# Performance work log

Measured on AMD Instinct MI355X. Metric: run time of the kernel, lower is better.

The kernel has to match this reference:

```python
import jax, jax.numpy as jnp
import numpy as np

NU, NS, NM = 80000, 20000, 30000
D = 128
E_UI, E_MM = 1_500_000, 480_000
B, L = 2048, 32
LAYERS = 2


def spmm(rows, cols, vals, x, n):
    # sparse [n,n] @ dense [n,d] via gather + segment_sum
    return jax.ops.segment_sum(vals[:, None] * x[cols], rows, num_segments=n)


def setup_inputs() -> dict:
    key = jax.random.key(0)
    ks = jax.random.split(key, 20)
    inp = {}
    inp['mashup_inputs'] = jax.random.randint(ks[0], (B,), 0, NM, dtype=jnp.int32)
    inp['service_inputs'] = jax.random.randint(ks[1], (B,), 0, NS, dtype=jnp.int32)
    inp['member_masked'] = jax.random.randint(ks[2], (B, L), 0, NU, dtype=jnp.int32)
    # variable-length compose lists: length in [1, L]; mask==1 marks padding
    lens = jax.random.randint(ks[3], (B, 1), 1, L + 1)
    inp['mask'] = (jnp.arange(L)[None, :] >= lens).astype(jnp.float32)
    inp['member_masked'] = jnp.where(inp['mask'] > 0, 0, inp['member_masked'])
    inp['adj_rows'] = jax.random.randint(ks[4], (E_UI,), 0, NU + NS, dtype=jnp.int32)
    inp['adj_cols'] = jax.random.randint(ks[5], (E_UI,), 0, NU + NS, dtype=jnp.int32)
    inp['adj_vals'] = jax.random.uniform(ks[6], (E_UI,)) * 0.1
    inp['A_rows'] = jax.random.randint(ks[7], (E_MM,), 0, NM, dtype=jnp.int32)
    inp['A_cols'] = jax.random.randint(ks[8], (E_MM,), 0, NM, dtype=jnp.int32)
    inp['A_vals'] = jax.random.uniform(ks[9], (E_MM,)) * 0.1
    inp['d_inv'] = jax.random.uniform(ks[10], (NM,)) * 0.1
    s = 0.05
    inp['user_tbl'] = jax.random.normal(ks[11], (NU, D)) * s
    inp['service_tbl'] = jax.random.normal(ks[12], (NS, D)) * s
    inp['mashup_tbl'] = jax.random.normal(ks[13], (NM, D)) * s
    inp['att_w1'] = jax.random.normal(ks[14], (2 * D, 16)) * s
    inp['att_b1'] = jnp.zeros((16,))
    inp['att_w2'] = jax.random.normal(ks[15], (16, 1)) * s
    inp['att_b2'] = jnp.zeros((1,))
    inp['pred_w1'] = jax.random.normal(ks[16], (3 * D, 8)) * s
    inp['pred_b1'] = jnp.zeros((8,))
    inp['pred_w2'] = jax.random.normal(ks[17], (8, 1)) * s
    inp['pred_b2'] = jnp.zeros((1,))
    return inp


def reference(mashup_inputs, service_inputs, member_masked, adj_rows, adj_cols,
              A_rows, A_cols, mask, user_tbl, service_tbl, mashup_tbl,
              adj_vals, A_vals, d_inv, att_w1, att_b1, att_w2, att_b2,
              pred_w1, pred_b1, pred_w2, pred_b2):
    # HyperConv on concatenated user+service embeddings (layer-mean aggregation)
    ui = jnp.concatenate([user_tbl, service_tbl], axis=0)  # [NU+NS, D]
    acc, h = ui, ui
    for _ in range(LAYERS):
        h = spmm(adj_rows, adj_cols, adj_vals, h, NU + NS)
        acc = acc + h
    ui = acc / (LAYERS + 1)
    user_e, service_e = ui[:NU], ui[NU:]
    service_emb = service_e[service_inputs]  # [B, D]

    # HyperConv2 on mashup graph: emb <- D^-1 A emb per layer, layer-mean
    acc, m = mashup_tbl, mashup_tbl
    for _ in range(LAYERS):
        m = d_inv[:, None] * spmm(A_rows, A_cols, A_vals, m, NM)
        acc = acc + m
    mashup_embedding = acc / (LAYERS + 1)

    # ragged gather + masked attention pooling over compose members
    member_emb = user_e[member_masked]                      # [B, L, D]
    svc_exp = jnp.broadcast_to(service_emb[:, None, :], (B, L, D))
    at_emb = jnp.concatenate([member_emb, svc_exp], axis=2)  # [B, L, 2D]
    hdn = jax.nn.relu(at_emb @ att_w1 + att_b1)             # [B, L, 16]
    scores = (hdn @ att_w2 + att_b2)[..., 0]                 # [B, L]
    scores = jnp.where(mask > 0, -1e9, scores)               # mask padding
    at_wt = jax.nn.softmax(scores, axis=1)
    g_att = jnp.einsum('bl,bld->bd', at_wt, member_emb)      # [B, D]

    mashup_emb = g_att + mashup_embedding[mashup_inputs]
    elem = mashup_emb * service_emb
    new_emb = jnp.concatenate([elem, mashup_emb, service_emb], axis=1)  # [B, 3D]
    hp = jax.nn.relu(new_emb @ pred_w1 + pred_b1)
    y = jax.nn.sigmoid(hp @ pred_w2 + pred_b2)               # [B, 1]
    return y
```

## Files before the change

kernel.cpp:

```cpp
#include <hip/hip_runtime.h>
#include <climits>

#define NU_ 80000
#define NS_ 20000
#define NM_ 30000
#define UIN_ (NU_ + NS_)
#define DD 128
#define LL 32
#define RPB 64
#define NCH 256
#define NBUK_UI ((UIN_ + RPB - 1) / RPB)
#define NBUK_MM ((NM_  + RPB - 1) / RPB)

#define F8_SCALE 512.0f
#define F8_INV   (1.0f / 512.0f)

typedef unsigned int   uint32;
typedef unsigned short ushort_t;
typedef unsigned char  uchar_t;
typedef float f32x2 __attribute__((ext_vector_type(2)));

__device__ __forceinline__ float bflo(uint32 u) { return __uint_as_float(u << 16); }
__device__ __forceinline__ float bfhi(uint32 u) { return __uint_as_float(u & 0xffff0000u); }
__device__ __forceinline__ uint32 f2bf(float f) {
    uint32 u = __float_as_uint(f);
    return (u + 0x7fffu + ((u >> 16) & 1u)) >> 16;
}
__device__ __forceinline__ uint32 pack2bf(float lo, float hi) {
    return f2bf(lo) | (f2bf(hi) << 16);
}

__device__ __forceinline__ float dec1_f8(uint32 b) {
    uint32 em = b & 0x7fu;
    uint32 s  = (b & 0x80u) << 24;
    float vn = __uint_as_float(s | (((em >> 3) + 120u) << 23) | ((em & 7u) << 20));
    float vd = (float)(int)em * 0.001953125f;
    vd = (b & 0x80u) ? -vd : vd;
    return (em >= 8u) ? vn : vd;
}
__device__ __forceinline__ uint32 enc1_f8(float f) {
    uint32 u = __float_as_uint(f);
    uint32 s = (u >> 31) << 7;
    float a = fabsf(f);
    if (a >= 448.0f) return s | 0x7Eu;
    if (a < 0.015625f) {
        int m = (int)(a * 512.0f + 0.5f);
        return s | (uint32)m;
    }
    uint32 au = u & 0x7fffffffu;
    au += 0x7FFFFu + ((au >> 20) & 1u);
    uint32 em = (((au >> 23) - 120u) << 3) | ((au >> 20) & 7u);
    if (em >= 0x7Fu) em = 0x7Eu;
    return s | em;
}
__device__ __forceinline__ f32x2 dec2_f8(uint32 u) {
#if __has_builtin(__builtin_amdgcn_cvt_pk_f32_fp8)
    return __builtin_amdgcn_cvt_pk_f32_fp8(u, false);
#else
    f32x2 r; r.x = dec1_f8(u & 0xffu); r.y = dec1_f8((u >> 8) & 0xffu); return r;
#endif
}
__device__ __forceinline__ f32x2 dec2_f8_hi(uint32 u) {
#if __has_builtin(__builtin_amdgcn_cvt_pk_f32_fp8)
    return __builtin_amdgcn_cvt_pk_f32_fp8(u, true);
#else
    f32x2 r; r.x = dec1_f8((u >> 16) & 0xffu); r.y = dec1_f8(u >> 24); return r;
#endif
}
__device__ __forceinline__ uint32 pack2f8(float lo, float hi) {
#if __has_builtin(__builtin_amdgcn_cvt_pk_fp8_f32)
    return (uint32)__builtin_amdgcn_cvt_pk_fp8_f32(lo, hi, 0, false) & 0xFFFFu;
#else
    return enc1_f8(lo) | (enc1_f8(hi) << 8);
#endif
}

__global__ void convert_kernel(const float* __restrict__ srcA, const float* __restrict__ srcB,
                               int split_rows, uint32* __restrict__ dst_bf,
                               ushort_t* __restrict__ dst_f8, size_t n2) {
    size_t stride = (size_t)gridDim.x * blockDim.x;
    const size_t split_e = (size_t)split_rows * DD;
    for (size_t i = (size_t)blockIdx.x * blockDim.x + threadIdx.x; i < n2; i += stride) {
        size_t e = i * 2;
        const float* s = (e < split_e) ? (srcA + e) : (srcB + (e - split_e));
        float2 v = *reinterpret_cast<const float2*>(s);
        dst_bf[i] = pack2bf(v.x, v.y);
        dst_f8[i] = (ushort_t)pack2f8(v.x * F8_SCALE, v.y * F8_SCALE);
    }
}

template <int NBUK>
__global__ __launch_bounds__(1024) void bucket_histA(const int* __restrict__ rows, int E,
                                                     int csz, int* __restrict__ h) {
    __shared__ int hist[NBUK];
    for (int i = threadIdx.x; i < NBUK; i += 1024) hist[i] = 0;
    __syncthreads();
    const int c  = blockIdx.x;
    const int lo = c * csz, hi = min(lo + csz, E);
    int i = lo + threadIdx.x;
    for (; i + 3 * 1024 < hi; i += 4 * 1024) {
        int r0 = rows[i];
        int r1 = rows[i + 1024];
        int r2 = rows[i + 2048];
        int r3 = rows[i + 3072];
        atomicAdd(&hist[r0 >> 6], 1);
        atomicAdd(&hist[r1 >> 6], 1);
        atomicAdd(&hist[r2 >> 6], 1);
        atomicAdd(&hist[r3 >> 6], 1);
    }
    for (; i < hi; i += 1024) atomicAdd(&hist[rows[i] >> 6], 1);
    __syncthreads();
    for (int b = threadIdx.x; b < NBUK; b += 1024)
        h[b * NCH + c] = hist[b];
}

__global__ __launch_bounds__(256) void scan_blocksum(const int* __restrict__ cnt,
                                                     int* __restrict__ bsum, int n) {
    __shared__ int red[256];
    int base = blockIdx.x * 1024 + threadIdx.x * 4;
    int s = 0;
    if (base + 3 < n) {
        int4 v = *reinterpret_cast<const int4*>(cnt + base);
        s = v.x + v.y + v.z + v.w;
    } else {
        for (int i = base; i < n && i < base + 4; ++i) s += cnt[i];
    }
    red[threadIdx.x] = s;
    __syncthreads();
    for (int off = 128; off >= 1; off >>= 1) {
        if (threadIdx.x < off) red[threadIdx.x] += red[threadIdx.x + off];
        __syncthreads();
    }
    if (threadIdx.x == 0) bsum[blockIdx.x] = red[0];
}

__global__ __launch_bounds__(256) void scan_final(const int* __restrict__ cnt,
                                                  const int* __restrict__ bsum,
                                                  int* __restrict__ row_ptr,
                                                  int* __restrict__ cursor, int n) {
    __shared__ int lds[256];
    __shared__ int blk_off_s;
    const int tid = threadIdx.x;
    const int b   = blockIdx.x;

    int s = 0;
    for (int j = tid; j < b; j += 256) s += bsum[j];
    lds[tid] = s;
    __syncthreads();
    for (int off = 128; off >= 1; off >>= 1) {
        if (tid < off) lds[tid] += lds[tid + off];
        __syncthreads();
    }
    if (tid == 0) blk_off_s = lds[0];
    __syncthreads();
    const int blk_off = blk_off_s;

    int base = b * 1024 + tid * 4;
    int c0 = 0, c1 = 0, c2 = 0, c3 = 0;
    if (base + 3 < n) {
        int4 v = *reinterpret_cast<const int4*>(cnt + base);
        c0 = v.x; c1 = v.y; c2 = v.z; c3 = v.w;
    } else {
        if (base     < n) c0 = cnt[base];
        if (base + 1 < n) c1 = cnt[base + 1];
        if (base + 2 < n) c2 = cnt[base + 2];
        if (base + 3 < n) c3 = cnt[base + 3];
    }
    int tsum = c0 + c1 + c2 + c3;
    __syncthreads();
    lds[tid] = tsum;
    __syncthreads();
    for (int off = 1; off < 256; off <<= 1) {
        int v = (tid >= off) ? lds[tid - off] : 0;
        __syncthreads();
        lds[tid] += v;
        __syncthreads();
    }
    int p0 = blk_off + ((tid > 0) ? lds[tid - 1] : 0);
    int p1 = p0 + c0, p2 = p1 + c1, p3 = p2 + c2, p4 = p3 + c3;

    if (base     < n) { row_ptr[base]     = p0; cursor[base]     = p0; if (base     == n - 1) row_ptr[n] = p1; }
    if (base + 1 < n) { row_ptr[base + 1] = p1; cursor[base + 1] = p1; if (base + 1 == n - 1) row_ptr[n] = p2; }
    if (base + 2 < n) { row_ptr[base + 2] = p2; cursor[base + 2] = p2; if (base + 2 == n - 1) row_ptr[n] = p3; }
    if (base + 3 < n) { row_ptr[base + 3] = p3; cursor[base + 3] = p3; if (base + 3 == n - 1) row_ptr[n] = p4; }
}

template <int NBUK>
__global__ __launch_bounds__(1024) void bucket_scatterA(
    const int* __restrict__ rows, const int* __restrict__ cols,
    const float* __restrict__ vals, const int* __restrict__ s,
    int E, int csz, uint2* __restrict__ cvA) {
    __shared__ int cur[NBUK];
    const int c = blockIdx.x;
    for (int b = threadIdx.x; b < NBUK; b += 1024) cur[b] = s[b * NCH + c];
    __syncthreads();
    const int lo = c * csz, hi = min(lo + csz, E);
    int i = lo + threadIdx.x;
    for (; i + 3 * 1024 < hi; i += 4 * 1024) {
        int   r0 = rows[i],        r1 = rows[i + 1024];
        int   r2 = rows[i + 2048], r3 = rows[i + 3072];
        int   q0 = cols[i],        q1 = cols[i + 1024];
        int   q2 = cols[i + 2048], q3 = cols[i + 3072];
        float v0 = vals[i],        v1 = vals[i + 1024];
        float v2 = vals[i + 2048], v3 = vals[i + 3072];
        int p0 = atomicAdd(&cur[r0 >> 6], 1);
        int p1 = atomicAdd(&cur[r1 >> 6], 1);
        int p2 = atomicAdd(&cur[r2 >> 6], 1);
        int p3 = atomicAdd(&cur[r3 >> 6], 1);
        cvA[p0] = make_uint2((uint32)q0 | ((uint32)(r0 & 63) << 25), __float_as_uint(v0));
        cvA[p1] = make_uint2((uint32)q1 | ((uint32)(r1 & 63) << 25), __float_as_uint(v1));
        cvA[p2] = make_uint2((uint32)q2 | ((uint32)(r2 & 63) << 25), __float_as_uint(v2));
        cvA[p3] = make_uint2((uint32)q3 | ((uint32)(r3 & 63) << 25), __float_as_uint(v3));
    }
    for (; i < hi; i += 1024) {
        int r = rows[i];
        int pos = atomicAdd(&cur[r >> 6], 1);
        cvA[pos] = make_uint2((uint32)cols[i] | ((uint32)(r & 63) << 25),
                              __float_as_uint(vals[i]));
    }
}

__global__ __launch_bounds__(256) void sort_bucket(
    const uint2* __restrict__ cvA, const int* __restrict__ s,
    uint2* __restrict__ cvB, int* __restrict__ row_ptr, int nrows) {
    __shared__ int cnt[RPB];
    __shared__ int cur[RPB];
    const int b    = blockIdx.x;
    const int tid  = threadIdx.x;
    const int base = s[b * NCH];
    const int endb = s[(b + 1) * NCH];

    if (tid < RPB) cnt[tid] = 0;
    __syncthreads();
    for (int i = base + tid; i < endb; i += 256)
        atomicAdd(&cnt[cvA[i].x >> 25], 1);
    __syncthreads();
    if (tid < 64) {
        int c = cnt[tid];
        int x = c;
        #pragma unroll
        for (int off = 1; off < 64; off <<= 1) {
            int v = __shfl_up(x, off);
            if (tid >= off) x += v;
        }
        int excl = base + x - c;
        cur[tid] = excl;
        int grow = b * RPB + tid;
        if (grow <= nrows) row_ptr[grow] = excl;
    }
    __syncthreads();
    for (int i = base + tid; i < endb; i += 256) {
        uint2 e = cvA[i];
        int rl  = (int)(e.x >> 25);
        int pos = atomicAdd(&cur[rl], 1);
        cvB[pos] = make_uint2(e.x & 0x1FFFFFFu, e.y);
    }
}

template <int MODE>
__global__ __launch_bounds__(256) void pull_kernel(
    const int* __restrict__ row_ptr, const uint2* __restrict__ cv,
    const uchar_t* __restrict__ x,
    const float* __restrict__ d_inv,
    const uint32* __restrict__ orig_bf, const uchar_t* __restrict__ hprev_f8,
    void* __restrict__ out, int n)
{
    const int wid  = (blockIdx.x * blockDim.x + threadIdx.x) >> 6;
    const int lane = threadIdx.x & 63;
    const int q    = lane >> 4;
    const int ql   = lane & 15;
    if (wid >= n) return;
    const int beg = row_ptr[wid];
    const int end = row_ptr[wid + 1];
    const int boff = ql << 3;

    float a0 = 0.f, a1 = 0.f, a2 = 0.f, a3 = 0.f;
    float a4 = 0.f, a5 = 0.f, a6 = 0.f, a7 = 0.f;

    int e = beg + q;
    for (; e + 4 < end; e += 8) {
        uint2 pa = cv[e];
        uint2 pb = cv[e + 4];
        uint2 ga = *reinterpret_cast<const uint2*>(x + (((size_t)pa.x) << 7) + boff);
        uint2 gb = *reinterpret_cast<const uint2*>(x + (((size_t)pb.x) << 7) + boff);
        float va = __uint_as_float(pa.y);
        float vb = __uint_as_float(pb.y);
        f32x2 d0 = dec2_f8(ga.x), d1 = dec2_f8_hi(ga.x);
        f32x2 d2 = dec2_f8(ga.y), d3 = dec2_f8_hi(ga.y);
        a0 += va * d0.x; a1 += va * d0.y; a2 += va * d1.x; a3 += va * d1.y;
        a4 += va * d2.x; a5 += va * d2.y; a6 += va * d3.x; a7 += va * d3.y;
        f32x2 e0 = dec2_f8(gb.x), e1 = dec2_f8_hi(gb.x);
        f32x2 e2 = dec2_f8(gb.y), e3 = dec2_f8_hi(gb.y);
        a0 += vb * e0.x; a1 += vb * e0.y; a2 += vb * e1.x; a3 += vb * e1.y;
        a4 += vb * e2.x; a5 += vb * e2.y; a6 += vb * e3.x; a7 += vb * e3.y;
    }
    if (e < end) {
        uint2 pa = cv[e];
        uint2 ga = *reinterpret_cast<const uint2*>(x + (((size_t)pa.x) << 7) + boff);
        float va = __uint_as_float(pa.y);
        f32x2 d0 = dec2_f8(ga.x), d1 = dec2_f8_hi(ga.x);
        f32x2 d2 = dec2_f8(ga.y), d3 = dec2_f8_hi(ga.y);
        a0 += va * d0.x; a1 += va * d0.y; a2 += va * d1.x; a3 += va * d1.y;
        a4 += va * d2.x; a5 += va * d2.y; a6 += va * d3.x; a7 += va * d3.y;
    }

    a0 += __shfl_xor(a0, 16); a0 += __shfl_xor(a0, 32);
    a1 += __shfl_xor(a1, 16); a1 += __shfl_xor(a1, 32);
    a2 += __shfl_xor(a2, 16); a2 += __shfl_xor(a2, 32);
    a3 += __shfl_xor(a3, 16); a3 += __shfl_xor(a3, 32);
    a4 += __shfl_xor(a4, 16); a4 += __shfl_xor(a4, 32);
    a5 += __shfl_xor(a5, 16); a5 += __shfl_xor(a5, 32);
    a6 += __shfl_xor(a6, 16); a6 += __shfl_xor(a6, 32);
    a7 += __shfl_xor(a7, 16); a7 += __shfl_xor(a7, 32);

    if (lane < 16) {
        if (MODE & 1) {
            float s = d_inv[wid];
            a0 *= s; a1 *= s; a2 *= s; a3 *= s;
            a4 *= s; a5 *= s; a6 *= s; a7 *= s;
        }
        if (MODE & 2) {
            const float inv3 = 1.0f / 3.0f;
            uint4 o = *reinterpret_cast<const uint4*>(orig_bf + (size_t)wid * 64 + (ql << 2));
            uint2 hp = *reinterpret_cast<const uint2*>(hprev_f8 + (((size_t)wid) << 7) + boff);
            f32x2 h0 = dec2_f8(hp.x), h1 = dec2_f8_hi(hp.x);
            f32x2 h2 = dec2_f8(hp.y), h3 = dec2_f8_hi(hp.y);
            uint4 r;
            r.x = pack2bf((bflo(o.x) + (h0.x + a0) * F8_INV) * inv3,
                          (bfhi(o.x) + (h0.y + a1) * F8_INV) * inv3);
            r.y = pack2bf((bflo(o.y) + (h1.x + a2) * F8_INV) * inv3,
                          (bfhi(o.y) + (h1.y + a3) * F8_INV) * inv3);
            r.z = pack2bf((bflo(o.z) + (h2.x + a4) * F8_INV) * inv3,
                          (bfhi(o.z) + (h2.y + a5) * F8_INV) * inv3);
            r.w = pack2bf((bflo(o.w) + (h3.x + a6) * F8_INV) * inv3,
                          (bfhi(o.w) + (h3.y + a7) * F8_INV) * inv3);
            *reinterpret_cast<uint4*>(reinterpret_cast<uint32*>(out) + (size_t)wid * 64 + (ql << 2)) = r;
        } else {
            uint2 r;
            r.x = pack2f8(a0, a1) | (pack2f8(a2, a3) << 16);
            r.y = pack2f8(a4, a5) | (pack2f8(a6, a7) << 16);
            *reinterpret_cast<uint2*>((uchar_t*)out + (((size_t)wid) << 7) + boff) = r;
        }
    }
}

__global__ __launch_bounds__(512) void attn_pred_kernel(
    const int* __restrict__ mashup_inputs, const int* __restrict__ service_inputs,
    const int* __restrict__ member_masked, const float* __restrict__ mask,
    const uint32* __restrict__ ui_final, const uint32* __restrict__ mash_final,
    const float* __restrict__ att_w1, const float* __restrict__ att_b1,
    const float* __restrict__ att_w2, const float* __restrict__ att_b2,
    const float* __restrict__ pred_w1, const float* __restrict__ pred_b1,
    const float* __restrict__ pred_w2, const float* __restrict__ pred_b2,
    float* __restrict__ out)
{
    const int b   = blockIdx.x;
    const int tid = threadIdx.x;

    __shared__ float mem_lds[LL * 129];
    __shared__ float svc_lds[DD];
    __shared__ float mash_lds[DD];
    __shared__ float w1_lds[2 * DD * 16];
    __shared__ float hdnw_lds[LL * 16];
    __shared__ float wt_lds[LL];
    __shared__ float new_lds[3 * DD];
    __shared__ float hp_lds[8];
    __shared__ int   midx[LL];

    if (tid < LL) midx[tid] = member_masked[b * LL + tid];
    for (int i = tid; i < 2 * DD * 16; i += 512) w1_lds[i] = att_w1[i];
    if (tid < 64) {
        int sidx = service_inputs[b];
        uint32 u = ui_final[(size_t)(NU_ + sidx) * 64 + tid];
        svc_lds[tid * 2]     = bflo(u);
        svc_lds[tid * 2 + 1] = bfhi(u);
    } else if (tid >= 448) {
        int t  = tid - 448;
        int mi = mashup_inputs[b];
        uint32 u = mash_final[(size_t)mi * 64 + t];
        mash_lds[t * 2]     = bflo(u);
        mash_lds[t * 2 + 1] = bfhi(u);
    }
    __syncthreads();

    for (int i = tid; i < LL * 64; i += 512) {
        int l = i >> 6, dp = (i & 63) * 2;
        uint32 u = ui_final[(size_t)midx[l] * 64 + (i & 63)];
        mem_lds[l * 129 + dp]     = bflo(u);
        mem_lds[l * 129 + dp + 1] = bfhi(u);
    }
    __syncthreads();

    {
        int l = tid >> 4, j = tid & 15;
        float acc = att_b1[j];
        const float* m = &mem_lds[l * 129];
        #pragma unroll 4
        for (int k = 0; k < DD; ++k) acc += m[k] * w1_lds[k * 16 + j];
        #pragma unroll 4
        for (int k = 0; k < DD; ++k) acc += svc_lds[k] * w1_lds[(DD + k) * 16 + j];
        acc = fmaxf(acc, 0.0f);
        hdnw_lds[l * 16 + j] = acc * att_w2[j];
    }
    __syncthreads();

    if (tid < 64) {
        float s = -3.0e38f;
        if (tid < LL) {
            s = att_b2[0];
            for (int j = 0; j < 16; ++j) s += hdnw_lds[tid * 16 + j];
            if (mask[b * LL + tid] > 0.0f) s = -1.0e9f;
        }
        float mx = s;
        for (int off = 16; off >= 1; off >>= 1) mx = fmaxf(mx, __shfl_xor(mx, off));
        float ex = (tid < LL) ? __expf(s - mx) : 0.0f;
        float sum = ex;
        for (int off = 16; off >= 1; off >>= 1) sum += __shfl_xor(sum, off);
        if (tid < LL) wt_lds[tid] = ex / sum;
    }
    __syncthreads();

    if (tid < DD) {
        float g = 0.0f;
        #pragma unroll 4
        for (int l = 0; l < LL; ++l) g += wt_lds[l] * mem_lds[l * 129 + tid];
        float me = g + mash_lds[tid];
        float sv = svc_lds[tid];
        new_lds[tid]          = me * sv;
        new_lds[DD + tid]     = me;
        new_lds[2 * DD + tid] = sv;
    }
    __syncthreads();

    if (tid < 8) {
        float acc = pred_b1[tid];
        for (int k = 0; k < 3 * DD; ++k) acc += new_lds[k] * pred_w1[k * 8 + tid];
        acc = fmaxf(acc, 0.0f);
        hp_lds[tid] = acc * pred_w2[tid];
    }
    __syncthreads();

    if (tid == 0) {
        float z = pred_b2[0];
        for (int j = 0; j < 8; ++j) z += hp_lds[j];
        out[b] = 1.0f / (1.0f + __expf(-z));
    }
}

extern "C" void kernel_launch(void* const* d_in, const int* in_sizes, int n_in,
                              void* d_out, int out_size, void* d_ws, size_t ws_size,
                              hipStream_t stream) {
    const int*   mashup_inputs  = (const int*)  d_in[0];
    const int*   service_inputs = (const int*)  d_in[1];
    const int*   member_masked  = (const int*)  d_in[2];
    const float* mask           = (const float*)d_in[3];
    const int*   adj_rows       = (const int*)  d_in[4];
    const int*   adj_cols       = (const int*)  d_in[5];
    const float* adj_vals       = (const float*)d_in[6];
    const int*   A_rows         = (const int*)  d_in[7];
    const int*   A_cols         = (const int*)  d_in[8];
    const float* A_vals         = (const float*)d_in[9];
    const float* d_inv          = (const float*)d_in[10];
    const float* user_tbl       = (const float*)d_in[11];
    const float* service_tbl    = (const float*)d_in[12];
    const float* mashup_tbl     = (const float*)d_in[13];
    const float* att_w1         = (const float*)d_in[14];
    const float* att_b1         = (const float*)d_in[15];
    const float* att_w2         = (const float*)d_in[16];
    const float* att_b2         = (const float*)d_in[17];
    const float* pred_w1        = (const float*)d_in[18];
    const float* pred_b1        = (const float*)d_in[19];
    const float* pred_w2        = (const float*)d_in[20];
    const float* pred_b2        = (const float*)d_in[21];

    const int E_ui = in_sizes[4];
    const int E_mm = in_sizes[7];
    const int B    = in_sizes[0];

    const int N_UI2  = NBUK_UI * NCH;
    const int N_MM2  = NBUK_MM * NCH;
    const int NB_UI  = (N_UI2 + 1023) / 1024;
    const int NB_MM  = (N_MM2 + 1023) / 1024;
    const int csz_ui = (E_ui + NCH - 1) / NCH;
    const int csz_mm = (E_mm + NCH - 1) / NCH;

    uint2*   cvA     = (uint2*)d_ws;
    uint2*   cvB_mm  = cvA + E_mm;
    uint2*   cvB_ui  = cvA + E_ui;
    int*     h_ui    = (int*)(cvB_ui + E_ui);
    int*     s_ui    = h_ui + N_UI2;
    int*     h_mm    = s_ui + N_UI2 + 4;
    int*     s_mm    = h_mm + N_MM2;
    int*     bs      = s_mm + N_MM2 + 4;
    int*     rp_ui   = bs + 512;
    int*     rp_mm   = rp_ui + UIN_ + 4;
    uint32*  ui_bf   = (uint32*)(rp_mm + NM_ + 4);
    uint32*  mash_bf = ui_bf + (size_t)UIN_ * 64;
    uint32*  h2      = mash_bf + (size_t)NM_ * 64;
    uint32*  m2      = h2 + (size_t)UIN_ * 64;
    uchar_t* ui_f8   = (uchar_t*)(m2 + (size_t)NM_ * 64);
    uchar_t* h1_f8   = ui_f8 + (size_t)UIN_ * DD;
    uchar_t* mash_f8 = h1_f8 + (size_t)UIN_ * DD;
    uchar_t* m1_f8   = mash_f8 + (size_t)NM_ * DD;

    convert_kernel<<<2048, 256, 0, stream>>>(user_tbl, service_tbl, NU_,
                                             ui_bf, (ushort_t*)ui_f8, (size_t)UIN_ * DD / 2);
    convert_kernel<<<1024, 256, 0, stream>>>(mashup_tbl, mashup_tbl, NM_,
                                             mash_bf, (ushort_t*)mash_f8, (size_t)NM_ * DD / 2);

    bucket_histA<NBUK_UI><<<NCH, 1024, 0, stream>>>(adj_rows, E_ui, csz_ui, h_ui);
    scan_blocksum<<<NB_UI, 256, 0, stream>>>(h_ui, bs, N_UI2);
    scan_final<<<NB_UI, 256, 0, stream>>>(h_ui, bs, s_ui, s_ui, N_UI2);
    bucket_scatterA<NBUK_UI><<<NCH, 1024, 0, stream>>>(adj_rows, adj_cols, adj_vals,
                                                       s_ui, E_ui, csz_ui, cvA);
    sort_bucket<<<NBUK_UI, 256, 0, stream>>>(cvA, s_ui, cvB_ui, rp_ui, UIN_);

    bucket_histA<NBUK_MM><<<NCH, 1024, 0, stream>>>(A_rows, E_mm, csz_mm, h_mm);
    scan_blocksum<<<NB_MM, 256, 0, stream>>>(h_mm, bs, N_MM2);
    scan_final<<<NB_MM, 256, 0, stream>>>(h_mm, bs, s_mm, s_mm, N_MM2);
    bucket_scatterA<NBUK_MM><<<NCH, 1024, 0, stream>>>(A_rows, A_cols, A_vals,
                                                       s_mm, E_mm, csz_mm, cvA);
    sort_bucket<<<NBUK_MM, 256, 0, stream>>>(cvA, s_mm, cvB_mm, rp_mm, NM_);

    const int ui_blocks = (UIN_ + 3) / 4;
    pull_kernel<0><<<ui_blocks, 256, 0, stream>>>(
        rp_ui, cvB_ui, ui_f8, nullptr, nullptr, nullptr, h1_f8, UIN_);
    pull_kernel<2><<<ui_blocks, 256, 0, stream>>>(
        rp_ui, cvB_ui, h1_f8, nullptr, ui_bf, h1_f8, h2, UIN_);

    const int mm_blocks = (NM_ + 3) / 4;
    pull_kernel<1><<<mm_blocks, 256, 0, stream>>>(
        rp_mm, cvB_mm, mash_f8, d_inv, nullptr, nullptr, m1_f8, NM_);
    pull_kernel<3><<<mm_blocks, 256, 0, stream>>>(
        rp_mm, cvB_mm, m1_f8, d_inv, mash_bf, m1_f8, m2, NM_);

    attn_pred_kernel<<<B, 512, 0, stream>>>(
        mashup_inputs, service_inputs, member_masked, mask,
        h2, m2,
        att_w1, att_b1, att_w2, att_b2,
        pred_w1, pred_b1, pred_w2, pred_b2,
        (float*)d_out);
}
```

Before: 261.8 us.

## Batch UI and mashup graph pipelines into shared fused kernel launches

```diff
diff --git a/kernel.cpp b/kernel.cpp
--- a/kernel.cpp
+++ b/kernel.cpp
@@ -75,27 +75,40 @@
 #endif
 }
 
-__global__ void convert_kernel(const float* __restrict__ srcA, const float* __restrict__ srcB,
-                               int split_rows, uint32* __restrict__ dst_bf,
-                               ushort_t* __restrict__ dst_f8, size_t n2) {
+__global__ void convert_fused(const float* __restrict__ user_tbl,
+                              const float* __restrict__ service_tbl,
+                              const float* __restrict__ mashup_tbl,
+                              uint32* __restrict__ ui_bf, ushort_t* __restrict__ ui_f8,
+                              uint32* __restrict__ mash_bf, ushort_t* __restrict__ mash_f8) {
+    const size_t P_UI = (size_t)UIN_ * 64;
+    const size_t P_MM = (size_t)NM_ * 64;
+    const size_t SPLIT = (size_t)NU_ * DD;
     size_t stride = (size_t)gridDim.x * blockDim.x;
-    const size_t split_e = (size_t)split_rows * DD;
-    for (size_t i = (size_t)blockIdx.x * blockDim.x + threadIdx.x; i < n2; i += stride) {
-        size_t e = i * 2;
-        const float* s = (e < split_e) ? (srcA + e) : (srcB + (e - split_e));
-        float2 v = *reinterpret_cast<const float2*>(s);
-        dst_bf[i] = pack2bf(v.x, v.y);
-        dst_f8[i] = (ushort_t)pack2f8(v.x * F8_SCALE, v.y * F8_SCALE);
-    }
-}
-
-template <int NBUK>
-__global__ __launch_bounds__(1024) void bucket_histA(const int* __restrict__ rows, int E,
-                                                     int csz, int* __restrict__ h) {
-    __shared__ int hist[NBUK];
-    for (int i = threadIdx.x; i < NBUK; i += 1024) hist[i] = 0;
-    __syncthreads();
-    const int c  = blockIdx.x;
+    for (size_t i = (size_t)blockIdx.x * blockDim.x + threadIdx.x; i < P_UI + P_MM; i += stride) {
+        if (i < P_UI) {
+            size_t e = i * 2;
+            const float* s = (e < SPLIT) ? (user_tbl + e) : (service_tbl + (e - SPLIT));
+            float2 v = *reinterpret_cast<const float2*>(s);
+            ui_bf[i] = pack2bf(v.x, v.y);
+            ui_f8[i] = (ushort_t)pack2f8(v.x * F8_SCALE, v.y * F8_SCALE);
+        } else {
+            size_t j = i - P_UI;
+            float2 v = *reinterpret_cast<const float2*>(mashup_tbl + j * 2);
+            mash_bf[j] = pack2bf(v.x, v.y);
+            mash_f8[j] = (ushort_t)pack2f8(v.x * F8_SCALE, v.y * F8_SCALE);
+        }
+    }
+}
+
+__global__ __launch_bounds__(1024) void hist_fused(
+    const int* __restrict__ rows_ui, int E_ui, int csz_ui, int* __restrict__ h_ui,
+    const int* __restrict__ rows_mm, int E_mm, int csz_mm, int* __restrict__ h_mm) {
+    __shared__ int hist[NBUK_UI];
+    const int* rows; int E, csz, nbuk, c; int* h;
+    if ((int)blockIdx.x < NCH) { rows = rows_ui; E = E_ui; csz = csz_ui; h = h_ui; nbuk = NBUK_UI; c = blockIdx.x; }
+    else                       { rows = rows_mm; E = E_mm; csz = csz_mm; h = h_mm; nbuk = NBUK_MM; c = blockIdx.x - NCH; }
+    for (int i = threadIdx.x; i < nbuk; i += 1024) hist[i] = 0;
+    __syncthreads();
     const int lo = c * csz, hi = min(lo + csz, E);
     int i = lo + threadIdx.x;
     for (; i + 3 * 1024 < hi; i += 4 * 1024) {
@@ -110,14 +123,18 @@
     }
     for (; i < hi; i += 1024) atomicAdd(&hist[rows[i] >> 6], 1);
     __syncthreads();
-    for (int b = threadIdx.x; b < NBUK; b += 1024)
+    for (int b = threadIdx.x; b < nbuk; b += 1024)
         h[b * NCH + c] = hist[b];
 }
 
-__global__ __launch_bounds__(256) void scan_blocksum(const int* __restrict__ cnt,
-                                                     int* __restrict__ bsum, int n) {
+__global__ __launch_bounds__(256) void scan_blocksum_fused(
+    const int* __restrict__ h_ui, int n_ui, int* __restrict__ bs_ui, int nb_ui,
+    const int* __restrict__ h_mm, int n_mm, int* __restrict__ bs_mm) {
     __shared__ int red[256];
-    int base = blockIdx.x * 1024 + threadIdx.x * 4;
+    const int* cnt; int n, b; int* bsum;
+    if ((int)blockIdx.x < nb_ui) { cnt = h_ui; n = n_ui; bsum = bs_ui; b = blockIdx.x; }
+    else                         { cnt = h_mm; n = n_mm; bsum = bs_mm; b = blockIdx.x - nb_ui; }
+    int base = b * 1024 + threadIdx.x * 4;
     int s = 0;
     if (base + 3 < n) {
         int4 v = *reinterpret_cast<const int4*>(cnt + base);
@@ -131,17 +148,20 @@
         if (threadIdx.x < off) red[threadIdx.x] += red[threadIdx.x + off];
         __syncthreads();
     }
-    if (threadIdx.x == 0) bsum[blockIdx.x] = red[0];
-}
-
-__global__ __launch_bounds__(256) void scan_final(const int* __restrict__ cnt,
-                                                  const int* __restrict__ bsum,
-                                                  int* __restrict__ row_ptr,
-                                                  int* __restrict__ cursor, int n) {
+    if (threadIdx.x == 0) bsum[b] = red[0];
+}
+
+__global__ __launch_bounds__(256) void scan_final_fused(
+    int* __restrict__ h_ui, int n_ui, const int* __restrict__ bs_ui, int nb_ui,
+    int* __restrict__ s_ui,
+    int* __restrict__ h_mm, int n_mm, const int* __restrict__ bs_mm,
+    int* __restrict__ s_mm) {
     __shared__ int lds[256];
     __shared__ int blk_off_s;
     const int tid = threadIdx.x;
-    const int b   = blockIdx.x;
+    int* cnt; int n, b; const int* bsum; int* row_ptr;
+    if ((int)blockIdx.x < nb_ui) { cnt = h_ui; n = n_ui; bsum = bs_ui; row_ptr = s_ui; b = blockIdx.x; }
+    else                         { cnt = h_mm; n = n_mm; bsum = bs_mm; row_ptr = s_mm; b = blockIdx.x - nb_ui; }
 
     int s = 0;
     for (int j = tid; j < b; j += 256) s += bsum[j];
@@ -179,20 +199,30 @@
     int p0 = blk_off + ((tid > 0) ? lds[tid - 1] : 0);
     int p1 = p0 + c0, p2 = p1 + c1, p3 = p2 + c2, p4 = p3 + c3;
 
-    if (base     < n) { row_ptr[base]     = p0; cursor[base]     = p0; if (base     == n - 1) row_ptr[n] = p1; }
-    if (base + 1 < n) { row_ptr[base + 1] = p1; cursor[base + 1] = p1; if (base + 1 == n - 1) row_ptr[n] = p2; }
-    if (base + 2 < n) { row_ptr[base + 2] = p2; cursor[base + 2] = p2; if (base + 2 == n - 1) row_ptr[n] = p3; }
-    if (base + 3 < n) { row_ptr[base + 3] = p3; cursor[base + 3] = p3; if (base + 3 == n - 1) row_ptr[n] = p4; }
-}
-
-template <int NBUK>
-__global__ __launch_bounds__(1024) void bucket_scatterA(
-    const int* __restrict__ rows, const int* __restrict__ cols,
-    const float* __restrict__ vals, const int* __restrict__ s,
-    int E, int csz, uint2* __restrict__ cvA) {
-    __shared__ int cur[NBUK];
-    const int c = blockIdx.x;
-    for (int b = threadIdx.x; b < NBUK; b += 1024) cur[b] = s[b * NCH + c];
+    if (base     < n) { row_ptr[base]     = p0; if (base     == n - 1) row_ptr[n] = p1; }
+    if (base + 1 < n) { row_ptr[base + 1] = p1; if (base + 1 == n - 1) row_ptr[n] = p2; }
+    if (base + 2 < n) { row_ptr[base + 2] = p2; if (base + 2 == n - 1) row_ptr[n] = p3; }
+    if (base + 3 < n) { row_ptr[base + 3] = p3; if (base + 3 == n - 1) row_ptr[n] = p4; }
+}
+
+__global__ __launch_bounds__(1024) void scatter_fused(
+    const int* __restrict__ rows_ui, const int* __restrict__ cols_ui,
+    const float* __restrict__ vals_ui, const int* __restrict__ s_ui,
+    int E_ui, int csz_ui, uint2* __restrict__ cvA_ui,
+    const int* __restrict__ rows_mm, const int* __restrict__ cols_mm,
+    const float* __restrict__ vals_mm, const int* __restrict__ s_mm,
+    int E_mm, int csz_mm, uint2* __restrict__ cvA_mm) {
+    __shared__ int cur[NBUK_UI];
+    const int *rows, *cols; const float* vals; const int* s;
+    int E, csz, nbuk, c; uint2* cvA;
+    if ((int)blockIdx.x < NCH) {
+        rows = rows_ui; cols = cols_ui; vals = vals_ui; s = s_ui;
+        E = E_ui; csz = csz_ui; nbuk = NBUK_UI; c = blockIdx.x; cvA = cvA_ui;
+    } else {
+        rows = rows_mm; cols = cols_mm; vals = vals_mm; s = s_mm;
+        E = E_mm; csz = csz_mm; nbuk = NBUK_MM; c = blockIdx.x - NCH; cvA = cvA_mm;
+    }
+    for (int b = threadIdx.x; b < nbuk; b += 1024) cur[b] = s[b * NCH + c];
     __syncthreads();
     const int lo = c * csz, hi = min(lo + csz, E);
     int i = lo + threadIdx.x;
@@ -220,12 +250,10 @@
     }
 }
 
-__global__ __launch_bounds__(256) void sort_bucket(
+__device__ __forceinline__ void sort_one_bucket(
     const uint2* __restrict__ cvA, const int* __restrict__ s,
-    uint2* __restrict__ cvB, int* __restrict__ row_ptr, int nrows) {
-    __shared__ int cnt[RPB];
-    __shared__ int cur[RPB];
-    const int b    = blockIdx.x;
+    uint2* __restrict__ cvB, int* __restrict__ row_ptr, int nrows, int b,
+    int* cnt, int* cur) {
     const int tid  = threadIdx.x;
     const int base = s[b * NCH];
     const int endb = s[(b + 1) * NCH];
@@ -257,44 +285,72 @@
     }
 }
 
+__global__ __launch_bounds__(256) void sort_fused(
+    const uint2* __restrict__ cvA_ui, const int* __restrict__ s_ui,
+    uint2* __restrict__ cvB_ui, int* __restrict__ rp_ui,
+    const uint2* __restrict__ cvA_mm, const int* __restrict__ s_mm,
+    uint2* __restrict__ cvB_mm, int* __restrict__ rp_mm) {
+    __shared__ int cnt[RPB];
+    __shared__ int cur[RPB];
+    if ((int)blockIdx.x < NBUK_UI)
+        sort_one_bucket(cvA_ui, s_ui, cvB_ui, rp_ui, UIN_, blockIdx.x, cnt, cur);
+    else
+        sort_one_bucket(cvA_mm, s_mm, cvB_mm, rp_mm, NM_, blockIdx.x - NBUK_UI, cnt, cur);
+}
+
 template <int MODE>
-__global__ __launch_bounds__(256) void pull_kernel(
+__device__ __forceinline__ void pull_row(
+    const int wid, const int lane,
     const int* __restrict__ row_ptr, const uint2* __restrict__ cv,
-    const uchar_t* __restrict__ x,
-    const float* __restrict__ d_inv,
+    const uchar_t* __restrict__ x, const float* __restrict__ d_inv,
     const uint32* __restrict__ orig_bf, const uchar_t* __restrict__ hprev_f8,
-    void* __restrict__ out, int n)
+    void* __restrict__ out)
 {
-    const int wid  = (blockIdx.x * blockDim.x + threadIdx.x) >> 6;
-    const int lane = threadIdx.x & 63;
     const int q    = lane >> 4;
     const int ql   = lane & 15;
-    if (wid >= n) return;
-    const int beg = row_ptr[wid];
-    const int end = row_ptr[wid + 1];
+    const int beg  = row_ptr[wid];
+    const int end  = row_ptr[wid + 1];
     const int boff = ql << 3;
 
     float a0 = 0.f, a1 = 0.f, a2 = 0.f, a3 = 0.f;
     float a4 = 0.f, a5 = 0.f, a6 = 0.f, a7 = 0.f;
 
     int e = beg + q;
-    for (; e + 4 < end; e += 8) {
-        uint2 pa = cv[e];
-        uint2 pb = cv[e + 4];
-        uint2 ga = *reinterpret_cast<const uint2*>(x + (((size_t)pa.x) << 7) + boff);
-        uint2 gb = *reinterpret_cast<const uint2*>(x + (((size_t)pb.x) << 7) + boff);
-        float va = __uint_as_float(pa.y);
-        float vb = __uint_as_float(pb.y);
-        f32x2 d0 = dec2_f8(ga.x), d1 = dec2_f8_hi(ga.x);
-        f32x2 d2 = dec2_f8(ga.y), d3 = dec2_f8_hi(ga.y);
-        a0 += va * d0.x; a1 += va * d0.y; a2 += va * d1.x; a3 += va * d1.y;
-        a4 += va * d2.x; a5 += va * d2.y; a6 += va * d3.x; a7 += va * d3.y;
-        f32x2 e0 = dec2_f8(gb.x), e1 = dec2_f8_hi(gb.x);
-        f32x2 e2 = dec2_f8(gb.y), e3 = dec2_f8_hi(gb.y);
-        a0 += vb * e0.x; a1 += vb * e0.y; a2 += vb * e1.x; a3 += vb * e1.y;
-        a4 += vb * e2.x; a5 += vb * e2.y; a6 += vb * e3.x; a7 += vb * e3.y;
-    }
-    if (e < end) {
+    for (; e + 12 < end; e += 16) {
+        uint2 p0 = cv[e],     p1 = cv[e + 4];
+        uint2 p2 = cv[e + 8], p3 = cv[e + 12];
+        uint2 g0 = *reinterpret_cast<const uint2*>(x + (((size_t)p0.x) << 7) + boff);
+        uint2 g1 = *reinterpret_cast<const uint2*>(x + (((size_t)p1.x) << 7) + boff);
+        uint2 g2 = *reinterpret_cast<const uint2*>(x + (((size_t)p2.x) << 7) + boff);
+        uint2 g3 = *reinterpret_cast<const uint2*>(x + (((size_t)p3.x) << 7) + boff);
+        float v0 = __uint_as_float(p0.y), v1 = __uint_as_float(p1.y);
+        float v2 = __uint_as_float(p2.y), v3 = __uint_as_float(p3.y);
+        {
+            f32x2 d0 = dec2_f8(g0.x), d1 = dec2_f8_hi(g0.x);
+            f32x2 d2 = dec2_f8(g0.y), d3 = dec2_f8_hi(g0.y);
+            a0 += v0 * d0.x; a1 += v0 * d0.y; a2 += v0 * d1.x; a3 += v0 * d1.y;
+            a4 += v0 * d2.x; a5 += v0 * d2.y; a6 += v0 * d3.x; a7 += v0 * d3.y;
+        }
+        {
+            f32x2 d0 = dec2_f8(g1.x), d1 = dec2_f8_hi(g1.x);
+            f32x2 d2 = dec2_f8(g1.y), d3 = dec2_f8_hi(g1.y);
+            a0 += v1 * d0.x; a1 += v1 * d0.y; a2 += v1 * d1.x; a3 += v1 * d1.y;
+            a4 += v1 * d2.x; a5 += v1 * d2.y; a6 += v1 * d3.x; a7 += v1 * d3.y;
+        }
+        {
+            f32x2 d0 = dec2_f8(g2.x), d1 = dec2_f8_hi(g2.x);
+            f32x2 d2 = dec2_f8(g2.y), d3 = dec2_f8_hi(g2.y);
+            a0 += v2 * d0.x; a1 += v2 * d0.y; a2 += v2 * d1.x; a3 += v2 * d1.y;
+            a4 += v2 * d2.x; a5 += v2 * d2.y; a6 += v2 * d3.x; a7 += v2 * d3.y;
+        }
+        {
+            f32x2 d0 = dec2_f8(g3.x), d1 = dec2_f8_hi(g3.x);
+            f32x2 d2 = dec2_f8(g3.y), d3 = dec2_f8_hi(g3.y);
+            a0 += v3 * d0.x; a1 += v3 * d0.y; a2 += v3 * d1.x; a3 += v3 * d1.y;
+            a4 += v3 * d2.x; a5 += v3 * d2.y; a6 += v3 * d3.x; a7 += v3 * d3.y;
+        }
+    }
+    for (; e < end; e += 4) {
         uint2 pa = cv[e];
         uint2 ga = *reinterpret_cast<const uint2*>(x + (((size_t)pa.x) << 7) + boff);
         float va = __uint_as_float(pa.y);
@@ -341,6 +397,47 @@
             r.y = pack2f8(a4, a5) | (pack2f8(a6, a7) << 16);
             *reinterpret_cast<uint2*>((uchar_t*)out + (((size_t)wid) << 7) + boff) = r;
         }
+    }
+}
+
+__global__ __launch_bounds__(256) void pull_L1_fused(
+    const int* __restrict__ rp_ui, const uint2* __restrict__ cv_ui,
+    const uchar_t* __restrict__ x_ui, uchar_t* __restrict__ out_ui,
+    const int* __restrict__ rp_mm, const uint2* __restrict__ cv_mm,
+    const uchar_t* __restrict__ x_mm, const float* __restrict__ d_inv,
+    uchar_t* __restrict__ out_mm, int ui_blocks)
+{
+    const int lane = threadIdx.x & 63;
+    const int w    = threadIdx.x >> 6;
+    if ((int)blockIdx.x < ui_blocks) {
+        int wid = blockIdx.x * 4 + w;
+        if (wid < UIN_)
+            pull_row<0>(wid, lane, rp_ui, cv_ui, x_ui, nullptr, nullptr, nullptr, out_ui);
+    } else {
+        int wid = (blockIdx.x - ui_blocks) * 4 + w;
+        if (wid < NM_)
+            pull_row<1>(wid, lane, rp_mm, cv_mm, x_mm, d_inv, nullptr, nullptr, out_mm);
+    }
+}
+
+__global__ __launch_bounds__(256) void pull_L2_fused(
+    const int* __restrict__ rp_ui, const uint2* __restrict__ cv_ui,
+    const uchar_t* __restrict__ h1_f8, const uint32* __restrict__ ui_bf,
+    uint32* __restrict__ h2,
+    const int* __restrict__ rp_mm, const uint2* __restrict__ cv_mm,
+    const uchar_t* __restrict__ m1_f8, const float* __restrict__ d_inv,
+    const uint32* __restrict__ mash_bf, uint32* __restrict__ m2, int ui_blocks)
+{
+    const int lane = threadIdx.x & 63;
+    const int w    = threadIdx.x >> 6;
+    if ((int)blockIdx.x < ui_blocks) {
+        int wid = blockIdx.x * 4 + w;
+        if (wid < UIN_)
+            pull_row<2>(wid, lane, rp_ui, cv_ui, h1_f8, nullptr, ui_bf, h1_f8, h2);
+    } else {
+        int wid = (blockIdx.x - ui_blocks) * 4 + w;
+        if (wid < NM_)
+            pull_row<3>(wid, lane, rp_mm, cv_mm, m1_f8, d_inv, mash_bf, m1_f8, m2);
     }
 }
 
@@ -484,15 +581,17 @@
     const int csz_ui = (E_ui + NCH - 1) / NCH;
     const int csz_mm = (E_mm + NCH - 1) / NCH;
 
-    uint2*   cvA     = (uint2*)d_ws;
-    uint2*   cvB_mm  = cvA + E_mm;
-    uint2*   cvB_ui  = cvA + E_ui;
-    int*     h_ui    = (int*)(cvB_ui + E_ui);
+    uint2*   cvA_ui  = (uint2*)d_ws;
+    uint2*   cvA_mm  = cvA_ui + E_ui;
+    uint2*   cvB_ui  = cvA_mm + E_mm;
+    uint2*   cvB_mm  = cvB_ui + E_ui;
+    int*     h_ui    = (int*)(cvB_mm + E_mm);
     int*     s_ui    = h_ui + N_UI2;
     int*     h_mm    = s_ui + N_UI2 + 4;
     int*     s_mm    = h_mm + N_MM2;
-    int*     bs      = s_mm + N_MM2 + 4;
-    int*     rp_ui   = bs + 512;
+    int*     bs_ui   = s_mm + N_MM2 + 4;
+    int*     bs_mm   = bs_ui + 512;
+    int*     rp_ui   = bs_mm + 128;
     int*     rp_mm   = rp_ui + UIN_ + 4;
     uint32*  ui_bf   = (uint32*)(rp_mm + NM_ + 4);
     uint32*  mash_bf = ui_bf + (size_t)UIN_ * 64;
@@ -503,36 +602,31 @@
     uchar_t* mash_f8 = h1_f8 + (size_t)UIN_ * DD;
     uchar_t* m1_f8   = mash_f8 + (size_t)NM_ * DD;
 
-    convert_kernel<<<2048, 256, 0, stream>>>(user_tbl, service_tbl, NU_,
-                                             ui_bf, (ushort_t*)ui_f8, (size_t)UIN_ * DD / 2);
-    convert_kernel<<<1024, 256, 0, stream>>>(mashup_tbl, mashup_tbl, NM_,
-                                             mash_bf, (ushort_t*)mash_f8, (size_t)NM_ * DD / 2);
-
-    bucket_histA<NBUK_UI><<<NCH, 1024, 0, stream>>>(adj_rows, E_ui, csz_ui, h_ui);
-    scan_blocksum<<<NB_UI, 256, 0, stream>>>(h_ui, bs, N_UI2);
-    scan_final<<<NB_UI, 256, 0, stream>>>(h_ui, bs, s_ui, s_ui, N_UI2);
-    bucket_scatterA<NBUK_UI><<<NCH, 1024, 0, stream>>>(adj_rows, adj_cols, adj_vals,
-                                                       s_ui, E_ui, csz_ui, cvA);
-    sort_bucket<<<NBUK_UI, 256, 0, stream>>>(cvA, s_ui, cvB_ui, rp_ui, UIN_);
-
-    bucket_histA<NBUK_MM><<<NCH, 1024, 0, stream>>>(A_rows, E_mm, csz_mm, h_mm);
-    scan_blocksum<<<NB_MM, 256, 0, stream>>>(h_mm, bs, N_MM2);
-    scan_final<<<NB_MM, 256, 0, stream>>>(h_mm, bs, s_mm, s_mm, N_MM2);
-    bucket_scatterA<NBUK_MM><<<NCH, 1024, 0, stream>>>(A_rows, A_cols, A_vals,
-                                                       s_mm, E_mm, csz_mm, cvA);
-    sort_bucket<<<NBUK_MM, 256, 0, stream>>>(cvA, s_mm, cvB_mm, rp_mm, NM_);
+    convert_fused<<<2048, 256, 0, stream>>>(user_tbl, service_tbl, mashup_tbl,
+                                            ui_bf, (ushort_t*)ui_f8,
+                                            mash_bf, (ushort_t*)mash_f8);
+
+    hist_fused<<<2 * NCH, 1024, 0, stream>>>(adj_rows, E_ui, csz_ui, h_ui,
+                                             A_rows, E_mm, csz_mm, h_mm);
+    scan_blocksum_fused<<<NB_UI + NB_MM, 256, 0, stream>>>(h_ui, N_UI2, bs_ui, NB_UI,
+                                                           h_mm, N_MM2, bs_mm);
+    scan_final_fused<<<NB_UI + NB_MM, 256, 0, stream>>>(h_ui, N_UI2, bs_ui, NB_UI, s_ui,
+                                                        h_mm, N_MM2, bs_mm, s_mm);
+    scatter_fused<<<2 * NCH, 1024, 0, stream>>>(
+        adj_rows, adj_cols, adj_vals, s_ui, E_ui, csz_ui, cvA_ui,
+        A_rows, A_cols, A_vals, s_mm, E_mm, csz_mm, cvA_mm);
+    sort_fused<<<NBUK_UI + NBUK_MM, 256, 0, stream>>>(
+        cvA_ui, s_ui, cvB_ui, rp_ui,
+        cvA_mm, s_mm, cvB_mm, rp_mm);
 
     const int ui_blocks = (UIN_ + 3) / 4;
-    pull_kernel<0><<<ui_blocks, 256, 0, stream>>>(
-        rp_ui, cvB_ui, ui_f8, nullptr, nullptr, nullptr, h1_f8, UIN_);
-    pull_kernel<2><<<ui_blocks, 256, 0, stream>>>(
-        rp_ui, cvB_ui, h1_f8, nullptr, ui_bf, h1_f8, h2, UIN_);
-
     const int mm_blocks = (NM_ + 3) / 4;
-    pull_kernel<1><<<mm_blocks, 256, 0, stream>>>(
-        rp_mm, cvB_mm, mash_f8, d_inv, nullptr, nullptr, m1_f8, NM_);
-    pull_kernel<3><<<mm_blocks, 256, 0, stream>>>(
-        rp_mm, cvB_mm, m1_f8, d_inv, mash_bf, m1_f8, m2, NM_);
+    pull_L1_fused<<<ui_blocks + mm_blocks, 256, 0, stream>>>(
+        rp_ui, cvB_ui, ui_f8, h1_f8,
+        rp_mm, cvB_mm, mash_f8, d_inv, m1_f8, ui_blocks);
+    pull_L2_fused<<<ui_blocks + mm_blocks, 256, 0, stream>>>(
+        rp_ui, cvB_ui, h1_f8, ui_bf, h2,
+        rp_mm, cvB_mm, m1_f8, d_inv, mash_bf, m2, ui_blocks);
 
     attn_pred_kernel<<<B, 512, 0, stream>>>(
         mashup_inputs, service_inputs, member_masked, mask,
```

New measurement: 262.8 us. No clear change (+0.4%).
